# Kernel tuning notes

Measured on AMD Instinct MI355X. Metric: run time of the kernel, lower is better.

The kernel has to match this reference:

```python
import jax, jax.numpy as jnp
import numpy as np

K = 16            # neighbors per node
NB = 8            # number_of_basis
MAX_RADIUS = 10.0
MUL_1E = 32       # multiplicity of the 1e output block
DIM_0E = 64       # 64x0e block (structurally zero: no 1o x 0e -> 0e path)
DIM_2E = 80       # 16x2e block (structurally zero: no 1o x 0e -> 2e path)


def knn_edges(coords):
    """coords [B,N,3] -> (senders, receivers) flat int32 indices of length B*N*K.
    Edge (j -> i): j is one of the K nearest neighbors of i (self excluded),
    matching torch_geometric knn_graph(loop=False, flow=source_to_target)."""
    B, N, _ = coords.shape
    n2 = jnp.sum(coords * coords, -1)                       # [B,N]
    d2 = n2[:, :, None] + n2[:, None, :] - 2.0 * jnp.einsum('bnd,bmd->bnm', coords, coords)
    d2 = d2 + jnp.eye(N, dtype=coords.dtype) * 1e10         # exclude self-loops
    _, idx = jax.lax.top_k(-d2, K)                          # [B,N,K] neighbor ids per node
    offs = (jnp.arange(B) * N)[:, None, None]
    senders = (idx + offs).reshape(-1)
    receivers = (jnp.broadcast_to(jnp.arange(N)[None, :, None], (B, N, K)) + offs).reshape(-1)
    return senders, receivers


def gaussian_soft_one_hot(x, number):
    # x in [0,1], shape [E,1] -> [E,number]
    centers = jnp.linspace(0.0, 1.0, number).astype(x.dtype)
    sigma = 1.0 / number
    g = jnp.exp(-(x - centers) ** 2 / (2.0 * sigma * sigma))
    s = jnp.sum(g, -1, keepdims=True)
    s = jnp.where(s > 0, s, jnp.ones_like(s))
    return g / s


def setup_inputs():
    key = jax.random.key(0)
    ks = jax.random.split(key, 6)
    B, N = 8, 4096
    coords = jax.random.normal(ks[0], (B, N, 3), dtype=jnp.float32) * 10.0
    atom_types = jax.random.randint(ks[1], (B, N), 0, 20)
    residue_types = jax.random.randint(ks[2], (B, N), 0, 21)
    tp_weight = jax.random.normal(ks[3], (NB, MUL_1E), dtype=jnp.float32) / np.sqrt(NB)
    atom_emb = jax.random.normal(ks[4], (20, 112), dtype=jnp.float32).at[0].set(0.0)   # padding_idx=0
    res_emb = jax.random.normal(ks[5], (21, 112), dtype=jnp.float32).at[0].set(0.0)    # padding_idx=0
    return {"coords": coords, "atom_types": atom_types, "residue_types": residue_types,
            "tp_weight": tp_weight, "atom_emb": atom_emb, "res_emb": res_emb}


def reference(coords, atom_types, residue_types, tp_weight, atom_emb, res_emb):
    B, N, _ = coords.shape
    E = B * N * K
    senders, receivers = knn_edges(coords)
    cf = coords.reshape(-1, 3)
    r = cf[senders] - cf[receivers]                           # [E,3]
    dist = jnp.linalg.norm(r, axis=-1, keepdims=True)         # [E,1]
    r_hat = r / (dist + 1e-8)
    cutoff = jnp.clip(dist / MAX_RADIUS, 0.0, 1.0)
    rb = gaussian_soft_one_hot(cutoff, NB)                    # [E,NB]
    # FullyConnectedTensorProduct(1x1o/1e, NBx0e -> ... 32x1e ...):
    feat_1e = jnp.einsum('ev,vw,em->ewm', rb, tp_weight, r_hat) / np.sqrt(3.0)  # [E,32,3]
    # scatter_mean over receivers
    num = jax.ops.segment_sum(feat_1e.reshape(E, MUL_1E * 3), receivers, num_segments=B * N)
    cnt = jax.ops.segment_sum(jnp.ones((E,), coords.dtype), receivers, num_segments=B * N)
    agg_1e = (num / jnp.maximum(cnt, 1.0)[:, None]).reshape(B, N, MUL_1E * 3)
    zeros0 = jnp.zeros((B, N, DIM_0E), coords.dtype)
    zeros2 = jnp.zeros((B, N, DIM_2E), coords.dtype)
    pos_feats = jnp.concatenate([zeros0, agg_1e, zeros2], -1)  # [B,N,240]
    node_features = jnp.concatenate([pos_feats, atom_emb[atom_types], res_emb[residue_types]], -1)
    return node_features  # [B,N,464]
```

## Files before the change

kernel.cpp:

```cpp
#include <hip/hip_runtime.h>
#include <hip/hip_bf16.h>

#define NN    4096
#define KNEI  16
#define QPW   4
#define WPB   16
#define BLOCK (WPB * 64)
#define QPB   (WPB * QPW)
#define BIGF  3.0e38f

typedef float f32x2 __attribute__((ext_vector_type(2)));

template<int CTRL>
__device__ __forceinline__ float dppmax_step(float f)
{
    int s_ = __builtin_amdgcn_update_dpp(__float_as_int(f), __float_as_int(f),
                                         CTRL, 0xF, 0xF, false);
    return fmaxf(f, __int_as_float(s_));
}

__device__ __forceinline__ float wave_max_dpp(float v)
{
    float f = v;
    f = dppmax_step<0x111>(f); f = dppmax_step<0x112>(f);
    f = dppmax_step<0x114>(f); f = dppmax_step<0x118>(f);
    f = dppmax_step<0x142>(f); f = dppmax_step<0x143>(f);
    return f;
}

__device__ __forceinline__ float row16_sum_dpp(float v)
{
    float f = v;
#define STEPA(CTRL)                                                          \
    { int s_ = __builtin_amdgcn_update_dpp(0, __float_as_int(f),             \
               (CTRL), 0xF, 0xF, true);                                      \
      f += __int_as_float(s_); }
    STEPA(0x111) STEPA(0x112) STEPA(0x114) STEPA(0x118)
#undef STEPA
    return f;
}

__device__ __forceinline__ int rlane(int v, int l)
{ return __builtin_amdgcn_readlane(v, l); }
__device__ __forceinline__ float rlanef(float v, int l)
{ return __int_as_float(__builtin_amdgcn_readlane(__float_as_int(v), l)); }

__device__ __forceinline__ void argmax_lite(float v, int idx,
                                            float& M, int& mi, int& w)
{
    M = rlanef(wave_max_dpp(v), 63);
    unsigned long long k = __ballot(v == M);
    w = __ffsll(k) - 1;
    mi = rlane(idx, w);
}

__device__ __forceinline__ void replay_fill(const float4* __restrict__ pts, int w,
    float xq, float yq, float zq, int qLoc, unsigned long long usedw, int lane,
    float& b, int& bi, float& s, int& si)
{
    int j2 = (lane << 6) | (w ^ lane);
    float4 P = pts[j2];
    float scr = fmaf(P.x, xq, fmaf(P.y, yq, fmaf(P.z, zq, P.w)));
    if (j2 == qLoc) scr = -BIGF;
    if ((usedw >> lane) & 1ull) scr = -BIGF;
    float M1; int i1, w1;
    argmax_lite(scr, j2, M1, i1, w1);
    if (lane == w1) scr = -BIGF;
    float M2; int i2, w2;
    argmax_lite(scr, j2, M2, i2, w2);
    if (lane == w) { b = M1; bi = i1; s = M2; si = i2; }
}

#define LADDER(d, b, bi, s, si)                                   \
    {  bool gtb = (d) > (b); bool gts = (d) > (s);                \
       (s)  = __builtin_amdgcn_fmed3f((d), (s), (b));             \
       (si) = gtb ? (bi) : (gts ? j : (si));                      \
       (b)  = fmaxf((b), (d));                                    \
       (bi) = gtb ? j : (bi); }

__global__ __launch_bounds__(BLOCK, 8)
void protein_enc_kernel(const float* __restrict__ coords,
                        const int*   __restrict__ atypes,
                        const int*   __restrict__ rtypes,
                        const float* __restrict__ tpw,
                        const float* __restrict__ aemb,
                        const float* __restrict__ remb,
                        float* __restrict__ out)
{
    __shared__ float4 pts[NN];
    __shared__ float  sW[8 * 32];

    const int tid  = threadIdx.x;
    const int lane = tid & 63;
    const int wv   = tid >> 6;
    const int bpb  = NN / QPB;
    const int batch    = blockIdx.x / bpb;
    const int nodeBase = (blockIdx.x % bpb) * QPB;

    const float* cb = coords + (size_t)batch * NN * 3;

    for (int p = tid; p < NN; p += BLOCK) {
        float x = cb[3*p], y = cb[3*p+1], z = cb[3*p+2];
        pts[p] = make_float4(x, y, z, -0.5f * (x*x + y*y + z*z));
    }
    if (tid < 256) sW[tid] = tpw[tid];
    __syncthreads();

    const int q0 = nodeBase + wv * QPW;
    const float4 P0 = pts[q0],   P1 = pts[q0+1];
    const float4 P2 = pts[q0+2], P3 = pts[q0+3];
    const float x0 = P0.x, y0 = P0.y, z0 = P0.z;
    const float x1 = P1.x, y1 = P1.y, z1 = P1.z;
    const float x2 = P2.x, y2 = P2.y, z2 = P2.z;
    const float x3 = P3.x, y3 = P3.y, z3 = P3.z;

    const f32x2 qAx = {x0, x1}, qAy = {y0, y1}, qAz = {z0, z1};
    const f32x2 qBx = {x2, x3}, qBy = {y2, y3}, qBz = {z2, z3};

    float b0 = -BIGF, s0 = -BIGF, b1 = -BIGF, s1 = -BIGF;
    float b2 = -BIGF, s2 = -BIGF, b3 = -BIGF, s3 = -BIGF;
    int bi0 = -1, si0 = -1, bi1 = -1, si1 = -1;
    int bi2 = -1, si2 = -1, bi3 = -1, si3 = -1;

    #pragma unroll 4
    for (int c = 0; c < NN / 64; ++c) {
        int j = (c << 6) | (lane ^ c);
        float4 P = pts[j];
        f32x2 Px = {P.x, P.x}, Py = {P.y, P.y}, Pz = {P.z, P.z}, Pw = {P.w, P.w};
        f32x2 dA = __builtin_elementwise_fma(Px, qAx,
                   __builtin_elementwise_fma(Py, qAy,
                   __builtin_elementwise_fma(Pz, qAz, Pw)));
        f32x2 dB = __builtin_elementwise_fma(Px, qBx,
                   __builtin_elementwise_fma(Py, qBy,
                   __builtin_elementwise_fma(Pz, qBz, Pw)));
        float d0 = dA.x, d1 = dA.y, d2 = dB.x, d3 = dB.y;
        LADDER(d0, b0, bi0, s0, si0)
        LADDER(d1, b1, bi1, s1, si1)
        LADDER(d2, b2, bi2, s2, si2)
        LADDER(d3, b3, bi3, s3, si3)
    }

    if (bi0 == q0  ) { b0 = s0; bi0 = si0; s0 = -BIGF; si0 = -1; }
    if (bi1 == q0+1) { b1 = s1; bi1 = si1; s1 = -BIGF; si1 = -1; }
    if (bi2 == q0+2) { b2 = s2; bi2 = si2; s2 = -BIGF; si2 = -1; }
    if (bi3 == q0+3) { b3 = s3; bi3 = si3; s3 = -BIGF; si3 = -1; }
    if (si0 == q0  ) { s0 = -BIGF; si0 = -1; }
    if (si1 == q0+1) { s1 = -BIGF; si1 = -1; }
    if (si2 == q0+2) { s2 = -BIGF; si2 = -1; }
    if (si3 == q0+3) { s3 = -BIGF; si3 = -1; }

    unsigned long long used0 = 0ull, used1 = 0ull, used2 = 0ull, used3 = 0ull;
    int selIdx = 0;

    #pragma unroll 1
    for (int r = 0; r < KNEI; ++r) {
        float f0 = b0, f1 = b1, f2 = b2, f3 = b3;
#define MS4(CTRL) f0 = dppmax_step<CTRL>(f0); f1 = dppmax_step<CTRL>(f1); \
                  f2 = dppmax_step<CTRL>(f2); f3 = dppmax_step<CTRL>(f3);
        MS4(0x111) MS4(0x112) MS4(0x114) MS4(0x118) MS4(0x142) MS4(0x143)
#undef MS4
        float M0 = rlanef(f0, 63), M1 = rlanef(f1, 63);
        float M2 = rlanef(f2, 63), M3 = rlanef(f3, 63);
        unsigned long long k0 = __ballot(b0 == M0), k1 = __ballot(b1 == M1);
        unsigned long long k2 = __ballot(b2 == M2), k3 = __ballot(b3 == M3);
        int w0 = __ffsll(k0) - 1, w1 = __ffsll(k1) - 1;
        int w2 = __ffsll(k2) - 1, w3 = __ffsll(k3) - 1;
        int mi0 = rlane(bi0, w0), mi1 = rlane(bi1, w1);
        int mi2 = rlane(bi2, w2), mi3 = rlane(bi3, w3);

        if (lane == r     ) selIdx = mi0;
        if (lane == r + 16) selIdx = mi1;
        if (lane == r + 32) selIdx = mi2;
        if (lane == r + 48) selIdx = mi3;

        bool n0 = rlane(si0, w0) == -1, n1 = rlane(si1, w1) == -1;
        bool n2 = rlane(si2, w2) == -1, n3 = rlane(si3, w3) == -1;

        if (lane == w0) { used0 |= 1ull << ((unsigned)(bi0 >> 6) & 63u);
                          b0 = s0; bi0 = si0; s0 = -BIGF; si0 = -1; }
        if (lane == w1) { used1 |= 1ull << ((unsigned)(bi1 >> 6) & 63u);
                          b1 = s1; bi1 = si1; s1 = -BIGF; si1 = -1; }
        if (lane == w2) { used2 |= 1ull << ((unsigned)(bi2 >> 6) & 63u);
                          b2 = s2; bi2 = si2; s2 = -BIGF; si2 = -1; }
        if (lane == w3) { used3 |= 1ull << ((unsigned)(bi3 >> 6) & 63u);
                          b3 = s3; bi3 = si3; s3 = -BIGF; si3 = -1; }

        if (n0 | n1 | n2 | n3) {
            if (n0) {
                unsigned long long uw =
                    ((unsigned long long)(unsigned)rlane((int)(used0 >> 32), w0) << 32)
                    | (unsigned)rlane((int)(used0 & 0xffffffffull), w0);
                replay_fill(pts, w0, x0, y0, z0, q0,   uw, lane, b0, bi0, s0, si0);
            }
            if (n1) {
                unsigned long long uw =
                    ((unsigned long long)(unsigned)rlane((int)(used1 >> 32), w1) << 32)
                    | (unsigned)rlane((int)(used1 & 0xffffffffull), w1);
                replay_fill(pts, w1, x1, y1, z1, q0+1, uw, lane, b1, bi1, s1, si1);
            }
            if (n2) {
                unsigned long long uw =
                    ((unsigned long long)(unsigned)rlane((int)(used2 >> 32), w2) << 32)
                    | (unsigned)rlane((int)(used2 & 0xffffffffull), w2);
                replay_fill(pts, w2, x2, y2, z2, q0+2, uw, lane, b2, bi2, s2, si2);
            }
            if (n3) {
                unsigned long long uw =
                    ((unsigned long long)(unsigned)rlane((int)(used3 >> 32), w3) << 32)
                    | (unsigned)rlane((int)(used3 & 0xffffffffull), w3);
                replay_fill(pts, w3, x3, y3, z3, q0+3, uw, lane, b3, bi3, s3, si3);
            }
        }
    }

    const int eq = lane >> 4;
    float xq = (eq & 2) ? ((eq & 1) ? x3 : x2) : ((eq & 1) ? x1 : x0);
    float yq = (eq & 2) ? ((eq & 1) ? y3 : y2) : ((eq & 1) ? y1 : y0);
    float zq = (eq & 2) ? ((eq & 1) ? z3 : z2) : ((eq & 1) ? z1 : z0);

    float4 P = pts[selIdx];
    float rx = P.x - xq, ry = P.y - yq, rz = P.z - zq;
    float dist = sqrtf(rx*rx + ry*ry + rz*rz);
    float inv  = 1.0f / (dist + 1e-8f);
    float hx = rx * inv, hy = ry * inv, hz = rz * inv;
    float cu = fminf(dist / 10.0f, 1.0f);
    float gg[8], ssum = 0.0f;
    #pragma unroll
    for (int v = 0; v < 8; ++v) {
        float d = cu - (float)v * (1.0f / 7.0f);
        gg[v] = expf(d * d * -32.0f);
        ssum += gg[v];
    }
    float is = 1.0f / ssum;
    float S[24];
    #pragma unroll
    for (int v = 0; v < 8; ++v) {
        float rbv = gg[v] * is;
        S[3*v]   = rbv * hx;
        S[3*v+1] = rbv * hy;
        S[3*v+2] = rbv * hz;
    }
    #pragma unroll
    for (int t = 0; t < 24; ++t) S[t] = row16_sum_dpp(S[t]);

    float wcol[8];
    #pragma unroll
    for (int v = 0; v < 8; ++v) wcol[v] = sW[32*v + (lane & 31)];

    const float scale = 0.036084391824351613f;
    const float4 z4 = make_float4(0.f, 0.f, 0.f, 0.f);

    #pragma unroll
    for (int q = 0; q < QPW; ++q) {
        const int gq = batch * NN + q0 + q;
        float sg[24];
        #pragma unroll
        for (int t = 0; t < 24; ++t) sg[t] = rlanef(S[t], 16 * q + 15);

        float* onode = out + (size_t)gq * 464;
        float4* o4 = (float4*)onode;
        if (lane < 16)       o4[lane] = z4;
        else if (lane < 36)  o4[lane + 24] = z4;

        if (lane < 32) {
            float a0 = 0.f, a1 = 0.f, a2 = 0.f;
            #pragma unroll
            for (int v = 0; v < 8; ++v) {
                a0 = fmaf(wcol[v], sg[3*v],   a0);
                a1 = fmaf(wcol[v], sg[3*v+1], a1);
                a2 = fmaf(wcol[v], sg[3*v+2], a2);
            }
            onode[64 + 3*lane]     = a0 * scale;
            onode[64 + 3*lane + 1] = a1 * scale;
            onode[64 + 3*lane + 2] = a2 * scale;
        }

        const int at = atypes[gq];
        const int rt = rtypes[gq];
        if (lane < 56) {
            float4 v = (lane < 28)
                ? ((const float4*)(aemb + 112*at))[lane]
                : ((const float4*)(remb + 112*rt))[lane - 28];
            o4[60 + lane] = v;
        }
    }
}

extern "C" void kernel_launch(void* const* d_in, const int* in_sizes, int n_in,
                              void* d_out, int out_size, void* d_ws, size_t ws_size,
                              hipStream_t stream)
{
    const float* coords = (const float*)d_in[0];
    const int*   at     = (const int*)  d_in[1];
    const int*   rt     = (const int*)  d_in[2];
    const float* tpw    = (const float*)d_in[3];
    const float* ae     = (const float*)d_in[4];
    const float* re     = (const float*)d_in[5];
    float* out = (float*)d_out;

    const int B = in_sizes[1] / NN;
    dim3 grid(B * (NN / QPB));
    protein_enc_kernel<<<grid, BLOCK, 0, stream>>>(coords, at, rt, tpw, ae, re, out);
}
```

Baseline: 90.74 us.

## Transpose per-column top-2 candidates into 16-lane rows for row-local argmax selection

After the distance scan, each query's 64 per-column best/second candidates are redistributed via ds_bpermute so each 16-lane row holds one query's candidates (4 per lane). The 16 selection rounds then use a row-local DPP argmax carrying the index, instead of four full-wave max+ballot+readlane chains per round. The replay path now rebuilds exclusions from the already-selected indices rather than per-column used bitmasks. This cuts cross-lane reduction work per round, at the cost of the up-front permutes, more live registers, and a heavier 16-iteration exclusion loop inside replay.

```diff
diff --git a/kernel.cpp b/kernel.cpp
--- a/kernel.cpp
+++ b/kernel.cpp
@@ -11,21 +11,35 @@
 
 typedef float f32x2 __attribute__((ext_vector_type(2)));
 
+__device__ __forceinline__ int rlane(int v, int l)
+{ return __builtin_amdgcn_readlane(v, l); }
+__device__ __forceinline__ float rlanef(float v, int l)
+{ return __int_as_float(__builtin_amdgcn_readlane(__float_as_int(v), l)); }
+
 template<int CTRL>
-__device__ __forceinline__ float dppmax_step(float f)
-{
-    int s_ = __builtin_amdgcn_update_dpp(__float_as_int(f), __float_as_int(f),
+__device__ __forceinline__ void amax_step(float& f, int& i)
+{
+    int fs = __builtin_amdgcn_update_dpp(__float_as_int(f), __float_as_int(f),
                                          CTRL, 0xF, 0xF, false);
-    return fmaxf(f, __int_as_float(s_));
-}
-
-__device__ __forceinline__ float wave_max_dpp(float v)
-{
-    float f = v;
-    f = dppmax_step<0x111>(f); f = dppmax_step<0x112>(f);
-    f = dppmax_step<0x114>(f); f = dppmax_step<0x118>(f);
-    f = dppmax_step<0x142>(f); f = dppmax_step<0x143>(f);
-    return f;
+    int is = __builtin_amdgcn_update_dpp(i, i, CTRL, 0xF, 0xF, false);
+    float ff = __int_as_float(fs);
+    bool gt = ff > f;
+    f = gt ? ff : f;
+    i = gt ? is : i;
+}
+
+__device__ __forceinline__ void wave_amax(float f, int i, float& M, int& mi)
+{
+    amax_step<0x111>(f, i); amax_step<0x112>(f, i); amax_step<0x114>(f, i);
+    amax_step<0x118>(f, i); amax_step<0x142>(f, i); amax_step<0x143>(f, i);
+    M  = rlanef(f, 63);
+    mi = rlane(i, 63);
+}
+
+__device__ __forceinline__ void row_amax(float& f, int& i)
+{
+    amax_step<0x121>(f, i); amax_step<0x122>(f, i);
+    amax_step<0x124>(f, i); amax_step<0x128>(f, i);
 }
 
 __device__ __forceinline__ float row16_sum_dpp(float v)
@@ -40,35 +54,22 @@
     return f;
 }
 
-__device__ __forceinline__ int rlane(int v, int l)
-{ return __builtin_amdgcn_readlane(v, l); }
-__device__ __forceinline__ float rlanef(float v, int l)
-{ return __int_as_float(__builtin_amdgcn_readlane(__float_as_int(v), l)); }
-
-__device__ __forceinline__ void argmax_lite(float v, int idx,
-                                            float& M, int& mi, int& w)
-{
-    M = rlanef(wave_max_dpp(v), 63);
-    unsigned long long k = __ballot(v == M);
-    w = __ffsll(k) - 1;
-    mi = rlane(idx, w);
-}
-
-__device__ __forceinline__ void replay_fill(const float4* __restrict__ pts, int w,
-    float xq, float yq, float zq, int qLoc, unsigned long long usedw, int lane,
-    float& b, int& bi, float& s, int& si)
-{
-    int j2 = (lane << 6) | (w ^ lane);
-    float4 P = pts[j2];
-    float scr = fmaf(P.x, xq, fmaf(P.y, yq, fmaf(P.z, zq, P.w)));
-    if (j2 == qLoc) scr = -BIGF;
-    if ((usedw >> lane) & 1ull) scr = -BIGF;
-    float M1; int i1, w1;
-    argmax_lite(scr, j2, M1, i1, w1);
-    if (lane == w1) scr = -BIGF;
-    float M2; int i2, w2;
-    argmax_lite(scr, j2, M2, i2, w2);
-    if (lane == w) { b = M1; bi = i1; s = M2; si = i2; }
+__device__ __forceinline__ float bpermf(int abyte, float v)
+{ return __int_as_float(__builtin_amdgcn_ds_bpermute(abyte, __float_as_int(v))); }
+__device__ __forceinline__ int bpermi(int abyte, int v)
+{ return __builtin_amdgcn_ds_bpermute(abyte, v); }
+
+__device__ __forceinline__ float sel4f(float a, float b, float c, float d, int q)
+{
+    float lo = (q & 1) ? b : a;
+    float hi = (q & 1) ? d : c;
+    return (q & 2) ? hi : lo;
+}
+__device__ __forceinline__ int sel4i(int a, int b, int c, int d, int q)
+{
+    int lo = (q & 1) ? b : a;
+    int hi = (q & 1) ? d : c;
+    return (q & 2) ? hi : lo;
 }
 
 #define LADDER(d, b, bi, s, si)                                   \
@@ -77,6 +78,43 @@
        (si) = gtb ? (bi) : (gts ? j : (si));                      \
        (b)  = fmaxf((b), (d));                                    \
        (bi) = gtb ? j : (bi); }
+
+#define REPLAY(q, xq, yq, zq)                                                \
+    {   int colq = rlane(col, 16 * (q));                                     \
+        int csq  = rlane(cs,  16 * (q));                                     \
+        int j2 = (lane << 6) | (colq ^ lane);                                \
+        float4 P = pts[j2];                                                  \
+        float scr = fmaf(P.x, (xq), fmaf(P.y, (yq), fmaf(P.z, (zq), P.w)));  \
+        if (j2 == q0 + (q)) scr = -BIGF;                                     \
+        _Pragma("unroll")                                                    \
+        for (int t = 0; t < KNEI; ++t) {                                     \
+            int sv = rlane(selIdx, 16 * (q) + t);                            \
+            if (j2 == sv) scr = -BIGF;                                       \
+        }                                                                    \
+        float M1; int i1;                                                    \
+        wave_amax(scr, j2, M1, i1);                                          \
+        float scr2 = (j2 == i1) ? -BIGF : scr;                               \
+        float M2; int i2;                                                    \
+        wave_amax(scr2, j2, M2, i2);                                         \
+        bool ow = (lane == 16 * (q) + (colq & 15));                          \
+        if (csq == 0) { pb0 = ow ? M1 : pb0; pbi0 = ow ? i1 : pbi0;          \
+                        ps0 = ow ? M2 : ps0; psi0 = ow ? i2 : psi0; }        \
+        else if (csq == 1) { pb1 = ow ? M1 : pb1; pbi1 = ow ? i1 : pbi1;     \
+                        ps1 = ow ? M2 : ps1; psi1 = ow ? i2 : psi1; }        \
+        else if (csq == 2) { pb2 = ow ? M1 : pb2; pbi2 = ow ? i1 : pbi2;     \
+                        ps2 = ow ? M2 : ps2; psi2 = ow ? i2 : psi2; }        \
+        else          { pb3 = ow ? M1 : pb3; pbi3 = ow ? i1 : pbi3;          \
+                        ps3 = ow ? M2 : ps3; psi3 = ow ? i2 : psi3; }        \
+    }
+
+#define PROMOTE(k, pb, pbi, ps, psi)                                         \
+    {   bool pk = own && (cs == (k));                                        \
+        exh = exh || (pk && ((psi) == -1));                                  \
+        (pb)  = pk ? (ps)  : (pb);                                           \
+        (pbi) = pk ? (psi) : (pbi);                                          \
+        (ps)  = pk ? -BIGF : (ps);                                           \
+        (psi) = pk ? -1    : (psi);                                          \
+    }
 
 __global__ __launch_bounds__(BLOCK, 8)
 void protein_enc_kernel(const float* __restrict__ coords,
@@ -149,74 +187,62 @@
     if (si2 == q0+2) { s2 = -BIGF; si2 = -1; }
     if (si3 == q0+3) { s3 = -BIGF; si3 = -1; }
 
-    unsigned long long used0 = 0ull, used1 = 0ull, used2 = 0ull, used3 = 0ull;
-    int selIdx = 0;
+    const int q = lane >> 4;
+    const int gt = lane & 15;
+    float pb0, pb1, pb2, pb3, ps0, ps1, ps2, ps3;
+    int   pbi0, pbi1, pbi2, pbi3, psi0, psi1, psi2, psi3;
+    {
+        const int ab = gt << 2;
+#define PULL(K, PB, PS, PBI, PSI)                                            \
+        {   int a = ab + ((K) << 6);                                         \
+            PB  = sel4f(bpermf(a,b0),  bpermf(a,b1),  bpermf(a,b2),  bpermf(a,b3),  q); \
+            PS  = sel4f(bpermf(a,s0),  bpermf(a,s1),  bpermf(a,s2),  bpermf(a,s3),  q); \
+            PBI = sel4i(bpermi(a,bi0), bpermi(a,bi1), bpermi(a,bi2), bpermi(a,bi3), q); \
+            PSI = sel4i(bpermi(a,si0), bpermi(a,si1), bpermi(a,si2), bpermi(a,si3), q); \
+        }
+        PULL(0, pb0, ps0, pbi0, psi0)
+        PULL(1, pb1, ps1, pbi1, psi1)
+        PULL(2, pb2, ps2, pbi2, psi2)
+        PULL(3, pb3, ps3, pbi3, psi3)
+#undef PULL
+    }
+
+    int selIdx = -1;
+    const int myR = gt;
 
     #pragma unroll 1
     for (int r = 0; r < KNEI; ++r) {
-        float f0 = b0, f1 = b1, f2 = b2, f3 = b3;
-#define MS4(CTRL) f0 = dppmax_step<CTRL>(f0); f1 = dppmax_step<CTRL>(f1); \
-                  f2 = dppmax_step<CTRL>(f2); f3 = dppmax_step<CTRL>(f3);
-        MS4(0x111) MS4(0x112) MS4(0x114) MS4(0x118) MS4(0x142) MS4(0x143)
-#undef MS4
-        float M0 = rlanef(f0, 63), M1 = rlanef(f1, 63);
-        float M2 = rlanef(f2, 63), M3 = rlanef(f3, 63);
-        unsigned long long k0 = __ballot(b0 == M0), k1 = __ballot(b1 == M1);
-        unsigned long long k2 = __ballot(b2 == M2), k3 = __ballot(b3 == M3);
-        int w0 = __ffsll(k0) - 1, w1 = __ffsll(k1) - 1;
-        int w2 = __ffsll(k2) - 1, w3 = __ffsll(k3) - 1;
-        int mi0 = rlane(bi0, w0), mi1 = rlane(bi1, w1);
-        int mi2 = rlane(bi2, w2), mi3 = rlane(bi3, w3);
-
-        if (lane == r     ) selIdx = mi0;
-        if (lane == r + 16) selIdx = mi1;
-        if (lane == r + 32) selIdx = mi2;
-        if (lane == r + 48) selIdx = mi3;
-
-        bool n0 = rlane(si0, w0) == -1, n1 = rlane(si1, w1) == -1;
-        bool n2 = rlane(si2, w2) == -1, n3 = rlane(si3, w3) == -1;
-
-        if (lane == w0) { used0 |= 1ull << ((unsigned)(bi0 >> 6) & 63u);
-                          b0 = s0; bi0 = si0; s0 = -BIGF; si0 = -1; }
-        if (lane == w1) { used1 |= 1ull << ((unsigned)(bi1 >> 6) & 63u);
-                          b1 = s1; bi1 = si1; s1 = -BIGF; si1 = -1; }
-        if (lane == w2) { used2 |= 1ull << ((unsigned)(bi2 >> 6) & 63u);
-                          b2 = s2; bi2 = si2; s2 = -BIGF; si2 = -1; }
-        if (lane == w3) { used3 |= 1ull << ((unsigned)(bi3 >> 6) & 63u);
-                          b3 = s3; bi3 = si3; s3 = -BIGF; si3 = -1; }
-
-        if (n0 | n1 | n2 | n3) {
-            if (n0) {
-                unsigned long long uw =
-                    ((unsigned long long)(unsigned)rlane((int)(used0 >> 32), w0) << 32)
-                    | (unsigned)rlane((int)(used0 & 0xffffffffull), w0);
-                replay_fill(pts, w0, x0, y0, z0, q0,   uw, lane, b0, bi0, s0, si0);
-            }
-            if (n1) {
-                unsigned long long uw =
-                    ((unsigned long long)(unsigned)rlane((int)(used1 >> 32), w1) << 32)
-                    | (unsigned)rlane((int)(used1 & 0xffffffffull), w1);
-                replay_fill(pts, w1, x1, y1, z1, q0+1, uw, lane, b1, bi1, s1, si1);
-            }
-            if (n2) {
-                unsigned long long uw =
-                    ((unsigned long long)(unsigned)rlane((int)(used2 >> 32), w2) << 32)
-                    | (unsigned)rlane((int)(used2 & 0xffffffffull), w2);
-                replay_fill(pts, w2, x2, y2, z2, q0+2, uw, lane, b2, bi2, s2, si2);
-            }
-            if (n3) {
-                unsigned long long uw =
-                    ((unsigned long long)(unsigned)rlane((int)(used3 >> 32), w3) << 32)
-                    | (unsigned)rlane((int)(used3 & 0xffffffffull), w3);
-                replay_fill(pts, w3, x3, y3, z3, q0+3, uw, lane, b3, bi3, s3, si3);
-            }
+        float f = pb0; int m = pbi0;
+        { bool g = pb1 > f; f = g ? pb1 : f; m = g ? ((1<<12)|pbi1) : m; }
+        { bool g = pb2 > f; f = g ? pb2 : f; m = g ? ((2<<12)|pbi2) : m; }
+        { bool g = pb3 > f; f = g ? pb3 : f; m = g ? ((3<<12)|pbi3) : m; }
+        row_amax(f, m);
+
+        int j   = m & 4095;
+        int cs  = m >> 12;
+        int col = (j & 63) ^ (j >> 6);
+        bool own = (myR == (col & 15));
+
+        if (myR == r) selIdx = j;
+
+        bool exh = false;
+        PROMOTE(0, pb0, pbi0, ps0, psi0)
+        PROMOTE(1, pb1, pbi1, ps1, psi1)
+        PROMOTE(2, pb2, pbi2, ps2, psi2)
+        PROMOTE(3, pb3, pbi3, ps3, psi3)
+
+        unsigned long long ex = __ballot(exh);
+        if (ex) {
+            if ((ex >>  0) & 0xFFFFull) REPLAY(0, x0, y0, z0)
+            if ((ex >> 16) & 0xFFFFull) REPLAY(1, x1, y1, z1)
+            if ((ex >> 32) & 0xFFFFull) REPLAY(2, x2, y2, z2)
+            if ((ex >> 48) & 0xFFFFull) REPLAY(3, x3, y3, z3)
         }
     }
 
-    const int eq = lane >> 4;
-    float xq = (eq & 2) ? ((eq & 1) ? x3 : x2) : ((eq & 1) ? x1 : x0);
-    float yq = (eq & 2) ? ((eq & 1) ? y3 : y2) : ((eq & 1) ? y1 : y0);
-    float zq = (eq & 2) ? ((eq & 1) ? z3 : z2) : ((eq & 1) ? z1 : z0);
+    float xq = (q & 2) ? ((q & 1) ? x3 : x2) : ((q & 1) ? x1 : x0);
+    float yq = (q & 2) ? ((q & 1) ? y3 : y2) : ((q & 1) ? y1 : y0);
+    float zq = (q & 2) ? ((q & 1) ? z3 : z2) : ((q & 1) ? z1 : z0);
 
     float4 P = pts[selIdx];
     float rx = P.x - xq, ry = P.y - yq, rz = P.z - zq;
@@ -251,11 +277,11 @@
     const float4 z4 = make_float4(0.f, 0.f, 0.f, 0.f);
 
     #pragma unroll
-    for (int q = 0; q < QPW; ++q) {
-        const int gq = batch * NN + q0 + q;
+    for (int qq = 0; qq < QPW; ++qq) {
+        const int gq = batch * NN + q0 + qq;
         float sg[24];
         #pragma unroll
-        for (int t = 0; t < 24; ++t) sg[t] = rlanef(S[t], 16 * q + 15);
+        for (int t = 0; t < 24; ++t) sg[t] = rlanef(S[t], 16 * qq + 15);
 
         float* onode = out + (size_t)gq * 464;
         float4* o4 = (float4*)onode;
```

Measured after the change: 85.42 us. 1.06x faster.
